# Optimization experiments

Measured on AMD Instinct MI355X. Metric: run time of the kernel, lower is better.

## Reference

```python
import jax, jax.numpy as jnp
import numpy as np

N_NODES = 20000
IN_CH = 7
HID = 256
HEADS = 8
NEG_SLOPE = 0.2


def glorot(key, shape):
    fan = shape[0] + shape[-1] if len(shape) == 2 else int(np.prod(shape))
    lim = jnp.sqrt(6.0 / fan)
    return jax.random.uniform(key, shape, jnp.float32, -lim, lim)


def setup_inputs() -> dict:
    key = jax.random.key(0)
    ks = jax.random.split(key, 12)
    x = jax.random.normal(ks[0], (N_NODES, IN_CH), jnp.float32)
    edge_index = jax.random.randint(ks[1], (2, 160000), 0, N_NODES, jnp.int64)
    # conv1: in=7 -> heads=8, out=256, concat
    W1 = glorot(ks[2], (IN_CH, HEADS * HID))
    att_src1 = glorot(ks[3], (HEADS, HID))
    att_dst1 = glorot(ks[4], (HEADS, HID))
    b1 = jnp.zeros((HEADS * HID,), jnp.float32)
    # conv2: in=2048 -> heads=1, out=256, mean (concat=False)
    W2 = glorot(ks[5], (HEADS * HID, 1 * HID))
    att_src2 = glorot(ks[6], (1, HID))
    att_dst2 = glorot(ks[7], (1, HID))
    b2 = jnp.zeros((HID,), jnp.float32)
    return {"x": x, "edge_index": edge_index, "W1": W1, "att_src1": att_src1,
            "att_dst1": att_dst1, "b1": b1, "W2": W2, "att_src2": att_src2,
            "att_dst2": att_dst2, "b2": b2}


def gat_conv(x, src, dst, W, att_src, att_dst, bias, concat):
    # PyG GATConv (eval mode, dropout disabled)
    H, C = att_src.shape
    n = x.shape[0]
    h = (x @ W).reshape(n, H, C)                      # [N,H,C]
    a_src = jnp.sum(h * att_src[None], axis=-1)       # [N,H]
    a_dst = jnp.sum(h * att_dst[None], axis=-1)       # [N,H]
    alpha = a_src[src] + a_dst[dst]                   # [E,H]
    alpha = jax.nn.leaky_relu(alpha, NEG_SLOPE)
    # segment softmax over incoming edges of each destination node
    amax = jax.ops.segment_max(alpha, dst, num_segments=n)
    alpha = jnp.exp(alpha - amax[dst])
    denom = jax.ops.segment_sum(alpha, dst, num_segments=n)
    alpha = alpha / (denom[dst] + 1e-16)
    msg = h[src] * alpha[:, :, None]                  # [E,H,C] gather + weight
    out = jax.ops.segment_sum(msg, dst, num_segments=n)  # scatter-add aggregate
    out = out.reshape(n, H * C) if concat else out.mean(axis=1)
    return out + bias


def reference(x, edge_index, W1, att_src1, att_dst1, b1, W2, att_src2, att_dst2, b2):
    n = x.shape[0]
    # PyG GATConv default: add self-loops
    loops = jnp.arange(n, dtype=edge_index.dtype)
    src = jnp.concatenate([edge_index[0], loops])
    dst = jnp.concatenate([edge_index[1], loops])
    h = gat_conv(x, src, dst, W1, att_src1, att_dst1, b1, concat=True)
    h = jax.nn.elu(h)
    out = gat_conv(h, src, dst, W2, att_src2, att_dst2, b2, concat=False)
    return out
```

## Files before the change

kernel.cpp:

```cpp
#include <hip/hip_runtime.h>
#include <hip/hip_bf16.h>

#define N_NODES 20000
#define E_ORIG  160000
#define E_TOT   180000
#define HEADS   8
#define HID     256
#define F1      2048
#define NEG     0.2f
#define MAXDEG  96
#define GBKS    32

typedef __attribute__((ext_vector_type(8))) short  short8;
typedef __attribute__((ext_vector_type(4))) short  short4_;
typedef __attribute__((ext_vector_type(4))) float  f32x4;

__device__ inline float bf2f(ushort u){ union{unsigned u32; float f;} v; v.u32=((unsigned)u)<<16; return v.f; }
__device__ inline ushort f2bf(float f){
  union{float f; unsigned u;} v; v.f=f;
  unsigned lsb=(v.u>>16)&1u; v.u += 0x7fffu + lsb; return (ushort)(v.u>>16);
}

__device__ inline void gload16(const ushort* g, ushort* s){
  __builtin_amdgcn_global_load_lds((const __attribute__((address_space(1))) unsigned int*)g,
                                   (__attribute__((address_space(3))) unsigned int*)s, 16, 0, 0);
}

__global__ __launch_bounds__(256) void k_pre(const float* __restrict__ x, const float* __restrict__ W1,
    const float* __restrict__ as1, const float* __restrict__ ad1, const float* __restrict__ W2,
    float* __restrict__ a_src1, float* __restrict__ a_dst1, ushort* __restrict__ W2bT,
    int* __restrict__ cnt){
  __shared__ float s_w[128];
  __shared__ ushort sh[256][65];
  int tid = threadIdx.x, bid = blockIdx.x;
  if (tid < 128){
    int t = tid & 63;
    int k = t>>3, i = t&7;
    float v = 0.f;
    if (i < 7){
      const float* wp = W1 + i*F1 + (k<<8);
      const float* ap = ((tid<64) ? as1 : ad1) + (k<<8);
      f32x4 a4 = {0,0,0,0};
      for (int c=0;c<256;c+=4)
        a4 += (*(const f32x4*)&wp[c]) * (*(const f32x4*)&ap[c]);
      v = a4[0]+a4[1]+a4[2]+a4[3];
    }
    s_w[tid] = v;
  }
  __syncthreads();
  {
    int nl = tid>>3, k = tid&7;
    int n = bid*32 + nl;
    if (n < N_NODES){
      float s=0.f, d=0.f;
      const float* ws = &s_w[k*8];
      const float* wd = &s_w[64+k*8];
#pragma unroll
      for (int i=0;i<7;i++){
        float xv = x[n*7+i];
        s += xv*ws[i]; d += xv*wd[i];
      }
      a_src1[n*8+k]=s; a_dst1[n*8+k]=d;
    }
  }
  if (bid >= 32 && bid < 111){
    int i = (bid-32)*256 + tid;
    if (i < N_NODES) cnt[i] = 0;
  }
  if (bid < 32){
    int k0 = bid*64;
    for (int kk=0; kk<64; kk++) sh[tid][kk] = f2bf(W2[(size_t)(k0+kk)*256 + tid]);
    __syncthreads();
#pragma unroll
    for (int c8=0; c8<8; c8++){
      short8 v;
#pragma unroll
      for (int j=0;j<8;j++) v[j] = (short)sh[tid][c8*8+j];
      *(short8*)&W2bT[(size_t)tid*F1 + k0 + c8*8] = v;
    }
  }
}

__global__ void k_scat(const int* __restrict__ ei, int* __restrict__ cnt, int* __restrict__ bucket){
  int e = blockIdx.x*256 + threadIdx.x;
  if (e >= E_TOT) return;
  int s, d;
  if (e < E_ORIG){ s = ei[e]; d = ei[E_ORIG + e]; }
  else           { s = d = e - E_ORIG; }
  int pos = atomicAdd(&cnt[d], 1);
  if (pos < MAXDEG) bucket[d*MAXDEG + pos] = s;
}

__global__ __launch_bounds__(512) void k_sa1(const int* __restrict__ cnt, const int* __restrict__ bucket,
    const float* __restrict__ a_src1, const float* __restrict__ a_dst1,
    const float* __restrict__ x, const float* __restrict__ W1, const float* __restrict__ b1,
    ushort* __restrict__ x2){
  __shared__ float sxa[8][64];
  int tid = threadIdx.x, wv = tid>>6, lane = tid&63;
  int n = blockIdx.x*8 + wv;
  {
    int k = lane>>3, i = lane&7;
    int ie = (i==7)?0:i;
    int base = n*MAXDEG;
    int deg  = cnt[n]; if (deg>MAXDEG) deg=MAXDEG;
    float ad = a_dst1[n*8+k];
    int src0 = (lane<deg)    ? bucket[base+lane]    : 0;
    int src1 = (lane+64<deg) ? bucket[base+lane+64] : 0;
    float denom = 0.f, acc = 0.f;
    int j = 0;
    for (; j+2<=deg; j+=2){
      int s0 = (j<64)   ? __shfl(src0,j)     : __shfl(src1,j-64);
      int s1 = (j+1<64) ? __shfl(src0,j+1)   : __shfl(src1,j-63);
      float A0 = a_src1[(size_t)s0*8+k] + ad;
      float A1 = a_src1[(size_t)s1*8+k] + ad;
      float X0 = x[(size_t)s0*7+ie];
      float X1 = x[(size_t)s1*7+ie];
      A0 = (A0>0.f)?A0:NEG*A0;  A1 = (A1>0.f)?A1:NEG*A1;
      float w0 = __expf(A0),   w1 = __expf(A1);
      denom += w0; acc += w0*X0;
      denom += w1; acc += w1*X1;
    }
    if (j<deg){
      int s0 = (j<64) ? __shfl(src0,j) : __shfl(src1,j-64);
      float A0 = a_src1[(size_t)s0*8+k] + ad;
      A0 = (A0>0.f)?A0:NEG*A0;
      float w0 = __expf(A0);
      denom += w0; acc += w0*x[(size_t)s0*7+ie];
    }
    sxa[wv][lane] = acc/denom;
  }
  __syncthreads();
  int kh = tid>>6, c4 = (tid&63)<<2;
  f32x4 w1r[7];
#pragma unroll
  for (int i=0;i<7;i++) w1r[i] = *(const f32x4*)(W1 + i*F1 + (kh<<8) + c4);
  f32x4 bb = *(const f32x4*)(b1 + (kh<<8) + c4);
#pragma unroll
  for (int g=0; g<8; g++){
    int nn = blockIdx.x*8 + g;
    const float* xa = &sxa[g][kh<<3];
    f32x4 h = bb;
#pragma unroll
    for (int i=0;i<7;i++) h += xa[i]*w1r[i];
    short4_ o;
#pragma unroll
    for (int j=0;j<4;j++){ float v=h[j]; v=(v>0.f)?v:(__expf(v)-1.f); o[j]=(short)f2bf(v); }
    *(short4_*)(x2 + (size_t)nn*F1 + (kh<<8) + c4) = o;
  }
}

__global__ __launch_bounds__(256,2) void k_gemm2m(const ushort* __restrict__ A,
    const ushort* __restrict__ BT, ushort* __restrict__ h2b,
    const float* __restrict__ as2, const float* __restrict__ ad2,
    float* __restrict__ a_src2, float* __restrict__ a_dst2){
  __shared__ __align__(16) ushort S[2][(64+256)*64];
  int tid = threadIdx.x;
  int m0 = blockIdx.x*64;
  int w = tid>>6, l = tid&63;
  int lrow = l&15, lk = l>>4;
  int nc = w<<6;

  const ushort* gp[10];
#pragma unroll
  for (int rep=0;rep<10;rep++){
    int lin = rep*256 + tid;
    if (lin < 512){
      int r = lin>>3, s = lin&7;
      int grow = m0 + r; if (grow >= N_NODES) grow = N_NODES-1;
      gp[rep] = A + (size_t)grow*F1 + ((s ^ (r&7))<<3);
    } else {
      int j = lin - 512;
      int c = j>>3, s = j&7;
      gp[rep] = BT + (size_t)c*F1 + ((s ^ (c&7))<<3);
    }
  }

  f32x4 acc[4][4] = {};

#pragma unroll
  for (int rep=0;rep<10;rep++) gload16(gp[rep], &S[0][(rep*256+tid)<<3]);
  __syncthreads();

  int cur = 0;
  for (int t=0; t<GBKS; t++){
    if (t+1 < GBKS){
      int k0 = (t+1)<<6;
#pragma unroll
      for (int rep=0;rep<10;rep++) gload16(gp[rep]+k0, &S[cur^1][(rep*256+tid)<<3]);
    }
    const ushort* as_ = &S[cur][0];
    const ushort* bs_ = &S[cur][4096];
#pragma unroll
    for (int kk=0;kk<2;kk++){
      short8 af[4], bfr[4];
#pragma unroll
      for (int m=0;m<4;m++){
        int r = (m<<4) + lrow;
        af[m] = *(const short8*)&as_[(r<<6) + ((((kk<<2)|lk) ^ (r&7))<<3)];
      }
#pragma unroll
      for (int n=0;n<4;n++){
        int c = nc + (n<<4) + lrow;
        bfr[n] = *(const short8*)&bs_[(c<<6) + ((((kk<<2)|lk) ^ (c&7))<<3)];
      }
#pragma unroll
      for (int m=0;m<4;m++)
#pragma unroll
        for (int n=0;n<4;n++)
          acc[m][n] = __builtin_amdgcn_mfma_f32_16x16x32_bf16(af[m], bfr[n], acc[m][n], 0,0,0);
    }
    __syncthreads();
    cur ^= 1;
  }

  float* sps = (float*)&S[0][0];
  float* spd = sps + 256;
  float s2v[4], d2v[4];
#pragma unroll
  for (int n=0;n<4;n++){
    int col = nc + (n<<4) + lrow;
    s2v[n]=as2[col]; d2v[n]=ad2[col];
  }
#pragma unroll
  for (int m=0;m<4;m++){
#pragma unroll
    for (int j=0;j<4;j++){
      int lrow64 = (m<<4) + (lk<<2) + j;
      int grow = m0 + lrow64;
      bool ok = grow < N_NODES;
      float ps=0.f, pd=0.f;
#pragma unroll
      for (int n=0;n<4;n++){
        float v = acc[m][n][j];
        ps += v*s2v[n]; pd += v*d2v[n];
        if (ok) h2b[(size_t)grow*256 + nc+(n<<4)+lrow] = f2bf(v);
      }
      ps += __shfl_xor(ps,8); ps += __shfl_xor(ps,4); ps += __shfl_xor(ps,2); ps += __shfl_xor(ps,1);
      pd += __shfl_xor(pd,8); pd += __shfl_xor(pd,4); pd += __shfl_xor(pd,2); pd += __shfl_xor(pd,1);
      if (lrow==0){
        sps[(lrow64<<2) | w] = ps;
        spd[(lrow64<<2) | w] = pd;
      }
    }
  }
  __syncthreads();
  if (tid < 64){
    int grow = m0 + tid;
    if (grow < N_NODES){
      f32x4 a = *(const f32x4*)&sps[tid<<2];
      f32x4 b = *(const f32x4*)&spd[tid<<2];
      a_src2[grow] = a[0]+a[1]+a[2]+a[3];
      a_dst2[grow] = b[0]+b[1]+b[2]+b[3];
    }
  }
}

__global__ __launch_bounds__(256) void k_agg2(const int* __restrict__ cnt, const int* __restrict__ bucket,
    const float* __restrict__ a_src2, const float* __restrict__ a_dst2, const ushort* __restrict__ h2b,
    const float* __restrict__ b2, float* __restrict__ out){
  int tid = threadIdx.x, wv = tid>>6, lane = tid&63;
  int n = blockIdx.x*4 + wv;
  int base = n*MAXDEG;
  int deg  = cnt[n]; if (deg > MAXDEG) deg = MAXDEG;
  float ad = a_dst2[n];

  int src0 = (lane<deg)     ? bucket[base+lane]    : 0;
  int src1 = (lane+64<deg)  ? bucket[base+lane+64] : 0;
  float a0 = -1e30f, a1 = -1e30f;
  if (lane<deg)   { float a = a_src2[src0]+ad; a0 = (a>0.f)?a:NEG*a; }
  if (lane+64<deg){ float a = a_src2[src1]+ad; a1 = (a>0.f)?a:NEG*a; }
  float m = fmaxf(a0,a1);
  for (int off=32; off; off>>=1) m = fmaxf(m, __shfl_xor(m,off));
  float e0 = (lane<deg)    ? __expf(a0-m) : 0.f;
  float e1 = (lane+64<deg) ? __expf(a1-m) : 0.f;
  float s = e0+e1;
  for (int off=32; off; off>>=1) s += __shfl_xor(s,off);
  float inv = 1.f/(s+1e-16f);
  e0 *= inv; e1 *= inv;

  int c0 = lane<<2;
  float acc0=0.f, acc1=0.f, acc2=0.f, acc3=0.f;
  int d1 = (deg<64)?deg:64;
  for (int j=0;j<d1;j++){
    float w = __shfl(e0, j);
    int  sj = __shfl(src0, j);
    short4_ hv = *(const short4_*)(h2b + (size_t)sj*256 + c0);
    acc0 += w*bf2f((ushort)hv[0]); acc1 += w*bf2f((ushort)hv[1]);
    acc2 += w*bf2f((ushort)hv[2]); acc3 += w*bf2f((ushort)hv[3]);
  }
  for (int j=64;j<deg;j++){
    float w = __shfl(e1, j-64);
    int  sj = __shfl(src1, j-64);
    short4_ hv = *(const short4_*)(h2b + (size_t)sj*256 + c0);
    acc0 += w*bf2f((ushort)hv[0]); acc1 += w*bf2f((ushort)hv[1]);
    acc2 += w*bf2f((ushort)hv[2]); acc3 += w*bf2f((ushort)hv[3]);
  }
  f32x4 bb = *(const f32x4*)(b2 + c0);
  f32x4 o; o[0]=acc0+bb[0]; o[1]=acc1+bb[1]; o[2]=acc2+bb[2]; o[3]=acc3+bb[3];
  *(f32x4*)(out + (size_t)n*256 + c0) = o;
}

extern "C" void kernel_launch(void* const* d_in, const int* in_sizes, int n_in,
                              void* d_out, int out_size, void* d_ws, size_t ws_size,
                              hipStream_t stream){
  const float* x      = (const float*)d_in[0];
  const int*   ei     = (const int*)  d_in[1];
  const float* W1     = (const float*)d_in[2];
  const float* att_s1 = (const float*)d_in[3];
  const float* att_d1 = (const float*)d_in[4];
  const float* b1     = (const float*)d_in[5];
  const float* W2     = (const float*)d_in[6];
  const float* att_s2 = (const float*)d_in[7];
  const float* att_d2 = (const float*)d_in[8];
  const float* b2     = (const float*)d_in[9];
  float* out = (float*)d_out;

  char* p = (char*)d_ws;
  auto alloc = [&](size_t bytes)->char*{ char* r = p; p += (bytes + 255) & ~(size_t)255; return r; };
  ushort* x2    = (ushort*)alloc((size_t)N_NODES*F1*2);
  ushort* W2bT  = (ushort*)alloc((size_t)F1*256*2);
  ushort* h2b   = (ushort*)alloc((size_t)N_NODES*256*2);
  float*  a_src1= (float*) alloc((size_t)N_NODES*8*4);
  float*  a_dst1= (float*) alloc((size_t)N_NODES*8*4);
  float*  a_src2= (float*) alloc((size_t)N_NODES*4);
  float*  a_dst2= (float*) alloc((size_t)N_NODES*4);
  int*    cnt   = (int*)   alloc((size_t)N_NODES*4);
  int*    bucket= (int*)   alloc((size_t)N_NODES*MAXDEG*4);

  k_pre    <<<(N_NODES+31)/32, 256, 0, stream>>>(x, W1, att_s1, att_d1, W2,
                                                 a_src1, a_dst1, W2bT, cnt);
  k_scat   <<<(E_TOT+255)/256, 256, 0, stream>>>(ei, cnt, bucket);
  k_sa1    <<<N_NODES/8, 512, 0, stream>>>(cnt, bucket, a_src1, a_dst1, x, W1, b1, x2);
  k_gemm2m <<<(N_NODES+63)/64, 256, 0, stream>>>(x2, W2bT, h2b, att_s2, att_d2, a_src2, a_dst2);
  k_agg2   <<<N_NODES/4, 256, 0, stream>>>(cnt, bucket, a_src2, a_dst2, h2b, b2, out);
}
```

Baseline: 121.9 us.

## Split GEMM2 output columns across two blocks with partial attention sums

The second-layer GEMM now gives each block a 64x128 tile instead of 64x256, which doubles the grid from 313 to 626 blocks and raises the occupancy hint to 3 blocks per CU. Because each block sees only half the columns, it writes partial a_src/a_dst dot products into two-slot arrays, and the aggregation kernel adds the two halves when it reads them. The aim is to fill more CUs and cut per-block shared memory. In exchange, each A tile is read from global memory twice, and the aggregation does extra reads of the partial sums.

```diff
diff --git a/kernel.cpp b/kernel.cpp
--- a/kernel.cpp
+++ b/kernel.cpp
@@ -14,6 +14,7 @@
 typedef __attribute__((ext_vector_type(8))) short  short8;
 typedef __attribute__((ext_vector_type(4))) short  short4_;
 typedef __attribute__((ext_vector_type(4))) float  f32x4;
+typedef __attribute__((ext_vector_type(2))) float  f32x2;
 
 __device__ inline float bf2f(ushort u){ union{unsigned u32; float f;} v; v.u32=((unsigned)u)<<16; return v.f; }
 __device__ inline ushort f2bf(float f){
@@ -149,20 +150,20 @@
   }
 }
 
-__global__ __launch_bounds__(256,2) void k_gemm2m(const ushort* __restrict__ A,
+__global__ __launch_bounds__(256,3) void k_gemm2m(const ushort* __restrict__ A,
     const ushort* __restrict__ BT, ushort* __restrict__ h2b,
     const float* __restrict__ as2, const float* __restrict__ ad2,
-    float* __restrict__ a_src2, float* __restrict__ a_dst2){
-  __shared__ __align__(16) ushort S[2][(64+256)*64];
-  int tid = threadIdx.x;
-  int m0 = blockIdx.x*64;
+    float* __restrict__ asrc_p, float* __restrict__ adst_p){
+  __shared__ __align__(16) ushort S[2][(64+128)*64];
+  int tid = threadIdx.x, bid = blockIdx.x;
+  int m0 = (bid>>1)*64, n0 = (bid&1)*128, nb = bid&1;
   int w = tid>>6, l = tid&63;
   int lrow = l&15, lk = l>>4;
-  int nc = w<<6;
-
-  const ushort* gp[10];
-#pragma unroll
-  for (int rep=0;rep<10;rep++){
+  int nc = w<<5;
+
+  const ushort* gp[6];
+#pragma unroll
+  for (int rep=0;rep<6;rep++){
     int lin = rep*256 + tid;
     if (lin < 512){
       int r = lin>>3, s = lin&7;
@@ -171,14 +172,14 @@
     } else {
       int j = lin - 512;
       int c = j>>3, s = j&7;
-      gp[rep] = BT + (size_t)c*F1 + ((s ^ (c&7))<<3);
-    }
-  }
-
-  f32x4 acc[4][4] = {};
-
-#pragma unroll
-  for (int rep=0;rep<10;rep++) gload16(gp[rep], &S[0][(rep*256+tid)<<3]);
+      gp[rep] = BT + (size_t)(n0+c)*F1 + ((s ^ (c&7))<<3);
+    }
+  }
+
+  f32x4 acc[4][2] = {};
+
+#pragma unroll
+  for (int rep=0;rep<6;rep++) gload16(gp[rep], &S[0][(rep*256+tid)<<3]);
   __syncthreads();
 
   int cur = 0;
@@ -186,27 +187,27 @@
     if (t+1 < GBKS){
       int k0 = (t+1)<<6;
 #pragma unroll
-      for (int rep=0;rep<10;rep++) gload16(gp[rep]+k0, &S[cur^1][(rep*256+tid)<<3]);
+      for (int rep=0;rep<6;rep++) gload16(gp[rep]+k0, &S[cur^1][(rep*256+tid)<<3]);
     }
     const ushort* as_ = &S[cur][0];
     const ushort* bs_ = &S[cur][4096];
 #pragma unroll
     for (int kk=0;kk<2;kk++){
-      short8 af[4], bfr[4];
+      short8 af[4], bfr[2];
 #pragma unroll
       for (int m=0;m<4;m++){
         int r = (m<<4) + lrow;
         af[m] = *(const short8*)&as_[(r<<6) + ((((kk<<2)|lk) ^ (r&7))<<3)];
       }
 #pragma unroll
-      for (int n=0;n<4;n++){
+      for (int n=0;n<2;n++){
         int c = nc + (n<<4) + lrow;
         bfr[n] = *(const short8*)&bs_[(c<<6) + ((((kk<<2)|lk) ^ (c&7))<<3)];
       }
 #pragma unroll
       for (int m=0;m<4;m++)
 #pragma unroll
-        for (int n=0;n<4;n++)
+        for (int n=0;n<2;n++)
           acc[m][n] = __builtin_amdgcn_mfma_f32_16x16x32_bf16(af[m], bfr[n], acc[m][n], 0,0,0);
     }
     __syncthreads();
@@ -215,31 +216,31 @@
 
   float* sps = (float*)&S[0][0];
   float* spd = sps + 256;
-  float s2v[4], d2v[4];
-#pragma unroll
-  for (int n=0;n<4;n++){
-    int col = nc + (n<<4) + lrow;
+  float s2v[2], d2v[2];
+#pragma unroll
+  for (int n=0;n<2;n++){
+    int col = n0 + nc + (n<<4) + lrow;
     s2v[n]=as2[col]; d2v[n]=ad2[col];
   }
 #pragma unroll
   for (int m=0;m<4;m++){
 #pragma unroll
     for (int j=0;j<4;j++){
-      int lrow64 = (m<<4) + (lk<<2) + j;
-      int grow = m0 + lrow64;
+      int lr = (m<<4) + (lk<<2) + j;
+      int grow = m0 + lr;
       bool ok = grow < N_NODES;
       float ps=0.f, pd=0.f;
 #pragma unroll
-      for (int n=0;n<4;n++){
+      for (int n=0;n<2;n++){
         float v = acc[m][n][j];
         ps += v*s2v[n]; pd += v*d2v[n];
-        if (ok) h2b[(size_t)grow*256 + nc+(n<<4)+lrow] = f2bf(v);
+        if (ok) h2b[(size_t)grow*256 + n0 + nc+(n<<4)+lrow] = f2bf(v);
       }
       ps += __shfl_xor(ps,8); ps += __shfl_xor(ps,4); ps += __shfl_xor(ps,2); ps += __shfl_xor(ps,1);
       pd += __shfl_xor(pd,8); pd += __shfl_xor(pd,4); pd += __shfl_xor(pd,2); pd += __shfl_xor(pd,1);
       if (lrow==0){
-        sps[(lrow64<<2) | w] = ps;
-        spd[(lrow64<<2) | w] = pd;
+        sps[(lr<<2) | w] = ps;
+        spd[(lr<<2) | w] = pd;
       }
     }
   }
@@ -249,26 +250,29 @@
     if (grow < N_NODES){
       f32x4 a = *(const f32x4*)&sps[tid<<2];
       f32x4 b = *(const f32x4*)&spd[tid<<2];
-      a_src2[grow] = a[0]+a[1]+a[2]+a[3];
-      a_dst2[grow] = b[0]+b[1]+b[2]+b[3];
+      asrc_p[(size_t)grow*2 + nb] = a[0]+a[1]+a[2]+a[3];
+      adst_p[(size_t)grow*2 + nb] = b[0]+b[1]+b[2]+b[3];
     }
   }
 }
 
 __global__ __launch_bounds__(256) void k_agg2(const int* __restrict__ cnt, const int* __restrict__ bucket,
-    const float* __restrict__ a_src2, const float* __restrict__ a_dst2, const ushort* __restrict__ h2b,
+    const float* __restrict__ asrc_p, const float* __restrict__ adst_p, const ushort* __restrict__ h2b,
     const float* __restrict__ b2, float* __restrict__ out){
   int tid = threadIdx.x, wv = tid>>6, lane = tid&63;
   int n = blockIdx.x*4 + wv;
   int base = n*MAXDEG;
   int deg  = cnt[n]; if (deg > MAXDEG) deg = MAXDEG;
-  float ad = a_dst2[n];
+  f32x2 adp = *(const f32x2*)(adst_p + (size_t)n*2);
+  float ad = adp[0] + adp[1];
 
   int src0 = (lane<deg)     ? bucket[base+lane]    : 0;
   int src1 = (lane+64<deg)  ? bucket[base+lane+64] : 0;
   float a0 = -1e30f, a1 = -1e30f;
-  if (lane<deg)   { float a = a_src2[src0]+ad; a0 = (a>0.f)?a:NEG*a; }
-  if (lane+64<deg){ float a = a_src2[src1]+ad; a1 = (a>0.f)?a:NEG*a; }
+  if (lane<deg)   { f32x2 sp = *(const f32x2*)(asrc_p + (size_t)src0*2);
+                    float a = sp[0]+sp[1]+ad; a0 = (a>0.f)?a:NEG*a; }
+  if (lane+64<deg){ f32x2 sp = *(const f32x2*)(asrc_p + (size_t)src1*2);
+                    float a = sp[0]+sp[1]+ad; a1 = (a>0.f)?a:NEG*a; }
   float m = fmaxf(a0,a1);
   for (int off=32; off; off>>=1) m = fmaxf(m, __shfl_xor(m,off));
   float e0 = (lane<deg)    ? __expf(a0-m) : 0.f;
@@ -322,8 +326,8 @@
   ushort* h2b   = (ushort*)alloc((size_t)N_NODES*256*2);
   float*  a_src1= (float*) alloc((size_t)N_NODES*8*4);
   float*  a_dst1= (float*) alloc((size_t)N_NODES*8*4);
-  float*  a_src2= (float*) alloc((size_t)N_NODES*4);
-  float*  a_dst2= (float*) alloc((size_t)N_NODES*4);
+  float*  asrc_p= (float*) alloc((size_t)N_NODES*2*4);
+  float*  adst_p= (float*) alloc((size_t)N_NODES*2*4);
   int*    cnt   = (int*)   alloc((size_t)N_NODES*4);
   int*    bucket= (int*)   alloc((size_t)N_NODES*MAXDEG*4);
 
@@ -331,6 +335,6 @@
                                                  a_src1, a_dst1, W2bT, cnt);
   k_scat   <<<(E_TOT+255)/256, 256, 0, stream>>>(ei, cnt, bucket);
   k_sa1    <<<N_NODES/8, 512, 0, stream>>>(cnt, bucket, a_src1, a_dst1, x, W1, b1, x2);
-  k_gemm2m <<<(N_NODES+63)/64, 256, 0, stream>>>(x2, W2bT, h2b, att_s2, att_d2, a_src2, a_dst2);
-  k_agg2   <<<N_NODES/4, 256, 0, stream>>>(cnt, bucket, a_src2, a_dst2, h2b, b2, out);
-}
+  k_gemm2m <<<((N_NODES+63)/64)*2, 256, 0, stream>>>(x2, W2bT, h2b, att_s2, att_d2, asrc_p, adst_p);
+  k_agg2   <<<N_NODES/4, 256, 0, stream>>>(cnt, bucket, asrc_p, adst_p, h2b, b2, out);
+}
```

Result: no change. 121.1 us (-0.7%).
